# Performance work log

Hardware: AMD Instinct MI355X
Metric: run time of the kernel (lower is better)

## Reference

```python
import jax, jax.numpy as jnp
import numpy as np

# Module hyperparameters (match init_kwargs)
C = 64      # in_channels
O = 256     # out_channels
K = 3       # filter_size
SUB = 2     # subsampling
SIGMA = 1.0
SCALE = 1.0 / SIGMA ** 2
EPS = 1e-8


def setup_inputs() -> dict:
    key = jax.random.key(0)
    k1, k2 = jax.random.split(key)
    x = jax.random.normal(k1, (32, C, 64, 64), dtype=jnp.float32)
    weight = jax.random.normal(k2, (O, C * K * K), dtype=jnp.float32)
    return {"x": x, "weight": weight}


def reference(x, weight):
    # Faithful to CKNLayer.forward, but expressed as a direct convolution
    # instead of materializing the im2col (unfold) tensor:
    #   unfold -> per-patch L2 norm -> (patches/norm) @ w_norm.T
    # == conv(x, w_norm) / patch_norm,   patch_norm = sqrt(conv(x^2, ones))
    B, _, H, W = x.shape
    pad = K // 2

    # F.normalize(weight, p=2, dim=1): clamp norm at 1e-12
    w_norm = weight / jnp.maximum(
        jnp.linalg.norm(weight, axis=1, keepdims=True), 1e-12
    )
    # torch unfold orders patch features as (c, kh, kw) -> reshape matches
    w4 = w_norm.reshape(O, C, K, K)

    dn = jax.lax.conv_dimension_numbers(x.shape, w4.shape, ('NCHW', 'OIHW', 'NCHW'))
    dots = jax.lax.conv_general_dilated(
        x, w4, window_strides=(1, 1), padding=[(pad, pad), (pad, pad)],
        dimension_numbers=dn)  # [B, O, H, W]

    ones_k = jnp.ones((1, C, K, K), x.dtype)
    sq = jax.lax.conv_general_dilated(
        x * x, ones_k, window_strides=(1, 1), padding=[(pad, pad), (pad, pad)],
        dimension_numbers=dn)  # [B, 1, H, W] = sum of squares per patch
    patch_norm = jnp.sqrt(jnp.maximum(sq, 0.0)) + EPS

    # Gaussian RBF on the unit sphere: exp(scale * (cos_sim - 1))
    out = jnp.exp(SCALE * (dots / patch_norm - 1.0))  # [B, O, H, W]

    # avg_pool2d(kernel=SUB, stride=SUB), H, W divisible by SUB
    out = out.reshape(B, O, H // SUB, SUB, W // SUB, SUB).mean(axis=(3, 5))
    return out
```

## Files before the change

### kernel.cpp

```cpp
#include <hip/hip_runtime.h>
#include <hip/hip_bf16.h>

typedef __attribute__((ext_vector_type(8))) short bf16x8;
typedef __attribute__((ext_vector_type(4))) float f32x4;
typedef __attribute__((ext_vector_type(16))) float f32x16;
typedef __attribute__((ext_vector_type(4))) unsigned u32x4;

__device__ __forceinline__ unsigned bfbits(float v) {
  __hip_bfloat16 h = __float2bfloat16(v);
  return (unsigned)*reinterpret_cast<unsigned short*>(&h);
}

__device__ __forceinline__ void wnorm_one(const float* __restrict__ w,
                                          ushort* __restrict__ wt,
                                          ushort* __restrict__ wt3,
                                          int o, int c) {
  float v[9];
  float ss = 0.f;
  const float* row = w + o * 576 + c * 9;
#pragma unroll
  for (int j = 0; j < 9; ++j) { v[j] = row[j]; ss += v[j] * v[j]; }
#pragma unroll
  for (int off = 32; off > 0; off >>= 1) ss += __shfl_xor(ss, off);
  const float inv = 1.0f / fmaxf(sqrtf(ss), 1e-12f);
  const int g = o >> 5, n = o & 31;
#pragma unroll
  for (int j = 0; j < 9; ++j) {
    const ushort bv = (ushort)bfbits(v[j] * inv);
    wt[o * 576 + j * 64 + c] = bv;
    const int ks = j * 4 + (c >> 4);
    wt3[((ks * 8 + g) * 32 + n) * 16 + (c & 15)] = bv;
  }
}

__global__ void wnorm_kernel(const float* __restrict__ w,
                             ushort* __restrict__ wt,
                             ushort* __restrict__ wt3) {
  wnorm_one(w, wt, wt3, blockIdx.x, threadIdx.x);
}

__global__ __launch_bounds__(256, 8) void xprep_kernel(
    const float* __restrict__ x, ushort* __restrict__ xt,
    float* __restrict__ css, const float* __restrict__ w,
    ushort* __restrict__ wt, ushort* __restrict__ wt3) {
  __shared__ __align__(16) unsigned tile[64 * 33];
  __shared__ __align__(16) float cssp[4 * 64];
  const int t = threadIdx.x;
  if (blockIdx.y == 32) {
    wnorm_one(w, wt, wt3, blockIdx.x * 4 + (t >> 6), t & 63);
    return;
  }
  const int y = blockIdx.x, b = blockIdx.y;
  const int c = t >> 2, m = t & 3;
  const int lane = t & 63, wv = t >> 6;

  const float* src = x + (((size_t)b * 64 + c) * 64 + y) * 64 + m * 4;
  float f[16];
#pragma unroll
  for (int j4 = 0; j4 < 4; ++j4) {
    const f32x4 v = *(const f32x4*)(src + j4 * 16);
#pragma unroll
    for (int k = 0; k < 4; ++k) f[j4 * 4 + k] = v[k];
  }
  float s[16];
#pragma unroll
  for (int j = 0; j < 16; ++j) {
    float v = f[j] * f[j];
    v += __shfl_xor(v, 4);
    v += __shfl_xor(v, 8);
    v += __shfl_xor(v, 16);
    v += __shfl_xor(v, 32);
    s[j] = v;
  }
  if (lane < 4) {
#pragma unroll
    for (int j4 = 0; j4 < 4; ++j4) {
      f32x4 v = {s[j4 * 4], s[j4 * 4 + 1], s[j4 * 4 + 2], s[j4 * 4 + 3]};
      *(f32x4*)(cssp + wv * 64 + j4 * 16 + lane * 4) = v;
    }
  }
  const int parity = c & 1;
  const int c2 = c >> 1;
#pragma unroll
  for (int j = 0; j < 16; ++j) {
    const float pf = __shfl_xor(f[j], 4);
    const bool mine = parity ? (j >= 8) : (j < 8);
    if (mine) {
      const unsigned dw = parity ? (bfbits(pf) | (bfbits(f[j]) << 16))
                                 : (bfbits(f[j]) | (bfbits(pf) << 16));
      const int px = (j >> 2) * 16 + m * 4 + (j & 3);
      tile[px * 33 + c2] = dw;
    }
  }
  __syncthreads();
  {
    const int xr = t & 63, q = t >> 6;
    unsigned d[8];
#pragma unroll
    for (int i = 0; i < 8; ++i) d[i] = tile[xr * 33 + q * 8 + i];
    ushort* dst =
        xt + ((((size_t)b * 64 + y) * 8 + 2 * q) * 64 + xr) * 8;
    u32x4 v0 = {d[0], d[1], d[2], d[3]};
    u32x4 v1 = {d[4], d[5], d[6], d[7]};
    *(u32x4*)dst = v0;
    *(u32x4*)(dst + 512) = v1;
  }
  if (t < 64) {
    const float sum = cssp[t] + cssp[64 + t] + cssp[128 + t] + cssp[192 + t];
    css[((size_t)b * 64 + y) * 64 + t] = sum;
  }
}

__global__ __launch_bounds__(512, 4) void ckn_main(
    const ushort* __restrict__ xt, const float* __restrict__ css,
    const ushort* __restrict__ wt3, float* __restrict__ out) {
  __shared__ __align__(16) char smem[67328];
  char* const xs = smem;
  float* const pool = (float*)(smem + 33792);
  float* const invp = (float*)(smem + 66816);
  const int PS = 258;

  const int tid = threadIdx.x;
  const int y0 = blockIdx.x;
  const int b = blockIdx.y;

  if (tid < 128) {
    const int ry = tid >> 6, xx = tid & 63;
    const int yc = 2 * y0 + ry;
    float s = 0.f;
#pragma unroll
    for (int dy = -1; dy <= 1; ++dy) {
      const int yy = yc + dy;
      if ((unsigned)yy < 64u) s += css[((size_t)b * 64 + yy) * 64 + xx];
    }
    const float sl = __shfl_up(s, 1);
    const float sr = __shfl_down(s, 1);
    const float tot = s + ((xx > 0) ? sl : 0.f) + ((xx < 63) ? sr : 0.f);
    invp[tid] = 1.0f / (sqrtf(fmaxf(tot, 0.f)) + 1e-8f);
  }

  if (tid < 64) {
    const int r4 = tid >> 4, cb = (tid >> 1) & 7, colsel = tid & 1;
    *(f32x4*)(xs + r4 * 8448 + cb * 1056 + colsel * 65 * 16) =
        (f32x4){0.f, 0.f, 0.f, 0.f};
  }

  {
    const int l = tid & 63;
    const int w = tid >> 6;
    const ushort* srcb = xt + (((size_t)b * 64) * 8 + w) * 512 + l * 8;
#pragma unroll
    for (int r4 = 0; r4 < 4; ++r4) {
      const int y_img = 2 * y0 - 1 + r4;
      char* dst = xs + r4 * 8448 + w * 1056 + (l + 1) * 16;
      if ((unsigned)y_img < 64u) {
        const ushort* src = srcb + (size_t)y_img * 4096;
        __builtin_amdgcn_global_load_lds(
            (const __attribute__((address_space(1))) void*)src,
            (__attribute__((address_space(3))) void*)dst, 16, 0, 0);
      } else {
        *(f32x4*)dst = (f32x4){0.f, 0.f, 0.f, 0.f};
      }
    }
  }

  const int lane = tid & 63;
  const int wid = tid >> 6;
  const int wave_m = wid & 1;
  const int wave_n = wid >> 1;
  const int lane31 = lane & 31;
  const int hi = lane >> 5;

  const ushort* wb3 = wt3 + (size_t)lane31 * 16 + hi * 8;
  const int g0 = wave_n * 2;

  bf16x8 bq[2][2];
#pragma unroll
  for (int nf = 0; nf < 2; ++nf) {
    bq[0][nf] = *(const bf16x8*)(wb3 + (size_t)(0 * 8 + g0 + nf) * 512);
    bq[1][nf] = *(const bf16x8*)(wb3 + (size_t)(1 * 8 + g0 + nf) * 512);
  }

  int PH[2][3];
#pragma unroll
  for (int mf = 0; mf < 2; ++mf)
#pragma unroll
    for (int kw = 0; kw < 3; ++kw)
      PH[mf][kw] =
          (mf * 32 + lane31 + kw) * 16 + hi * 1056 + wave_m * 8448;

  __syncthreads();

  f32x16 acc[2][2];
#pragma unroll
  for (int i = 0; i < 2; ++i)
#pragma unroll
    for (int j = 0; j < 2; ++j)
#pragma unroll
      for (int e = 0; e < 16; ++e) acc[i][j][e] = 0.f;

#pragma unroll
  for (int ks = 0; ks < 36; ++ks) {
    const int t9 = ks >> 2;
    const int kh = t9 / 3, kw = t9 % 3;
    const int stepoff = kh * 8448 + (ks & 3) * 2112;
    const int cur = ks & 1;
    bf16x8 afrag[2];
#pragma unroll
    for (int mf = 0; mf < 2; ++mf)
      afrag[mf] = *(const bf16x8*)(xs + PH[mf][kw] + stepoff);
    __builtin_amdgcn_s_setprio(1);
#pragma unroll
    for (int mf = 0; mf < 2; ++mf)
#pragma unroll
      for (int nf = 0; nf < 2; ++nf)
        acc[mf][nf] = __builtin_amdgcn_mfma_f32_32x32x16_bf16(
            afrag[mf], bq[cur][nf], acc[mf][nf], 0, 0, 0);
    __builtin_amdgcn_s_setprio(0);
    if (ks + 2 < 36) {
#pragma unroll
      for (int nf = 0; nf < 2; ++nf)
        bq[cur][nf] =
            *(const bf16x8*)(wb3 + (size_t)((ks + 2) * 8 + g0 + nf) * 512);
    }
  }

  if (wave_m == 1) {
#pragma unroll
    for (int mf = 0; mf < 2; ++mf)
#pragma unroll
      for (int q = 0; q < 4; ++q) {
        const f32x4 ip = *(const f32x4*)(invp + 64 + mf * 32 + 8 * q + 4 * hi);
        const int px = mf * 16 + 4 * q + 2 * hi;
#pragma unroll
        for (int nf = 0; nf < 2; ++nf) {
          const int o = wave_n * 64 + nf * 32 + lane31;
          const float e0 = __expf(acc[mf][nf][4 * q + 0] * ip[0] - 1.f);
          const float e1 = __expf(acc[mf][nf][4 * q + 1] * ip[1] - 1.f);
          const float e2 = __expf(acc[mf][nf][4 * q + 2] * ip[2] - 1.f);
          const float e3 = __expf(acc[mf][nf][4 * q + 3] * ip[3] - 1.f);
          pool[px * PS + o] = e0 + e1;
          pool[(px + 1) * PS + o] = e2 + e3;
        }
      }
  }
  __syncthreads();
  if (wave_m == 0) {
#pragma unroll
    for (int mf = 0; mf < 2; ++mf)
#pragma unroll
      for (int q = 0; q < 4; ++q) {
        const f32x4 ip = *(const f32x4*)(invp + mf * 32 + 8 * q + 4 * hi);
        const int px = mf * 16 + 4 * q + 2 * hi;
#pragma unroll
        for (int nf = 0; nf < 2; ++nf) {
          const int o = wave_n * 64 + nf * 32 + lane31;
          const float e0 = __expf(acc[mf][nf][4 * q + 0] * ip[0] - 1.f);
          const float e1 = __expf(acc[mf][nf][4 * q + 1] * ip[1] - 1.f);
          const float e2 = __expf(acc[mf][nf][4 * q + 2] * ip[2] - 1.f);
          const float e3 = __expf(acc[mf][nf][4 * q + 3] * ip[3] - 1.f);
          pool[px * PS + o] = 0.25f * (pool[px * PS + o] + e0 + e1);
          pool[(px + 1) * PS + o] = 0.25f * (pool[(px + 1) * PS + o] + e2 + e3);
        }
      }
  }
  __syncthreads();

  const size_t obase = (((size_t)b * 256) * 32 + y0) * 32;
#pragma unroll
  for (int j = 0; j < 4; ++j) {
    const int o = j * 64 + (tid >> 3);
    const int ch = (tid & 7) * 4;
    const f32x4 v = {pool[(ch + 0) * PS + o], pool[(ch + 1) * PS + o],
                     pool[(ch + 2) * PS + o], pool[(ch + 3) * PS + o]};
    *(f32x4*)(out + obase + (size_t)o * 1024 + ch) = v;
  }
}

__global__ __launch_bounds__(512, 4) void ckn_main_v1(
    const float* __restrict__ x, const ushort* __restrict__ wt,
    float* __restrict__ out) {
  __shared__ __align__(16) char smem[43552];
  char* const xs = smem;
  float* const invp = (float*)(smem + 33792);
  float* const cs = (float*)(smem + 34304);
  float* const csp = (float*)(smem + 35360);
  float* const pool = (float*)smem;

  const int tid = threadIdx.x;
  const int y0 = blockIdx.x;
  const int b = blockIdx.y;

  if (tid < 64) {
    const int r4 = tid >> 4, colsel = (tid >> 3) & 1, cblk = tid & 7;
    const int col = colsel * 65;
    *(f32x4*)(xs + r4 * 8448 + col * 128 + cblk * 16) =
        (f32x4){0.f, 0.f, 0.f, 0.f};
  }
  {
    const int xx = tid & 63;
    const int cg = tid >> 6;
    const int col = xx + 1;
    const int sw = (cg * 16) ^ ((col & 7) << 4);
#pragma unroll
    for (int r4 = 0; r4 < 4; ++r4) {
      const int y_img = 2 * y0 - 1 + r4;
      char* dst = xs + r4 * 8448 + col * 128 + sw;
      if ((unsigned)y_img < 64u) {
        const float* src =
            x + (((size_t)b * 64 + cg * 8) * 64 + y_img) * 64 + xx;
        float ss = 0.f;
        union { bf16x8 v; ushort u[8]; } pk;
#pragma unroll
        for (int j = 0; j < 8; ++j) {
          const float f = src[(size_t)j * 4096];
          ss += f * f;
          pk.u[j] = (ushort)bfbits(f);
        }
        *(bf16x8*)dst = pk.v;
        csp[(r4 * 8 + cg) * 64 + xx] = ss;
      } else {
        *(bf16x8*)dst = (bf16x8){0, 0, 0, 0, 0, 0, 0, 0};
        csp[(r4 * 8 + cg) * 64 + xx] = 0.f;
      }
    }
  }
  __syncthreads();
  if (tid < 256) {
    const int r4 = tid >> 6, xc = tid & 63;
    float s = 0.f;
#pragma unroll
    for (int cg = 0; cg < 8; ++cg) s += csp[(r4 * 8 + cg) * 64 + xc];
    cs[r4 * 66 + xc + 1] = s;
  }
  if (tid >= 256 && tid < 264) {
    const int t = tid - 256;
    cs[(t >> 1) * 66 + (t & 1) * 65] = 0.f;
  }
  __syncthreads();
  if (tid < 128) {
    const int ry = tid >> 6, xp = tid & 63;
    float s = 0.f;
#pragma unroll
    for (int dr = 0; dr < 3; ++dr)
#pragma unroll
      for (int dc = 0; dc < 3; ++dc) s += cs[(ry + dr) * 66 + xp + dc];
    invp[tid] = 1.0f / (sqrtf(fmaxf(s, 0.f)) + 1e-8f);
  }
  __syncthreads();

  const int lane = tid & 63;
  const int wid = tid >> 6;
  const int wave_m = wid & 1;
  const int wave_n = wid >> 1;
  const int lane16 = lane & 15;
  const int klane = lane >> 4;
  const int o_base = wave_n * 64;

  f32x4 acc[4][4];
#pragma unroll
  for (int i = 0; i < 4; ++i)
#pragma unroll
    for (int j = 0; j < 4; ++j) acc[i][j] = (f32x4){0.f, 0.f, 0.f, 0.f};
  const ushort* wbase = wt + (o_base + lane16) * 576 + klane * 8;
#pragma unroll
  for (int ks = 0; ks < 18; ++ks) {
    const int t9 = ks >> 1;
    const int kh = t9 / 3, kw = t9 % 3;
    const int cb = (ks & 1) * 64 + klane * 16;
    bf16x8 bfrag[4];
#pragma unroll
    for (int fn = 0; fn < 4; ++fn)
      bfrag[fn] = *(const bf16x8*)(wbase + fn * 16 * 576 + ks * 32);
    const int r4 = wave_m + kh;
#pragma unroll
    for (int fm = 0; fm < 4; ++fm) {
      const int col = fm * 16 + lane16 + kw;
      const int addr = r4 * 8448 + col * 128 + (cb ^ ((col & 7) << 4));
      const bf16x8 afrag = *(const bf16x8*)(xs + addr);
#pragma unroll
      for (int fn = 0; fn < 4; ++fn)
        acc[fm][fn] = __builtin_amdgcn_mfma_f32_16x16x32_bf16(
            afrag, bfrag[fn], acc[fm][fn], 0, 0, 0);
    }
  }
  float ep0[4][4], ep1[4][4];
#pragma unroll
  for (int fm = 0; fm < 4; ++fm) {
    const int m = wave_m * 64 + fm * 16 + klane * 4;
    const f32x4 ip = *(const f32x4*)(invp + m);
#pragma unroll
    for (int fn = 0; fn < 4; ++fn) {
      const f32x4 v = acc[fm][fn];
      const float e0 = __expf(v[0] * ip[0] - 1.f);
      const float e1 = __expf(v[1] * ip[1] - 1.f);
      const float e2 = __expf(v[2] * ip[2] - 1.f);
      const float e3 = __expf(v[3] * ip[3] - 1.f);
      ep0[fm][fn] = e0 + e1;
      ep1[fm][fn] = e2 + e3;
    }
  }
  __syncthreads();
  if (wave_m == 1) {
#pragma unroll
    for (int fm = 0; fm < 4; ++fm) {
      const int ox = fm * 8 + klane * 2;
#pragma unroll
      for (int fn = 0; fn < 4; ++fn) {
        const int o = o_base + fn * 16 + lane16;
        *(float2*)(pool + o * 32 + ox) = make_float2(ep0[fm][fn], ep1[fm][fn]);
      }
    }
  }
  __syncthreads();
  if (wave_m == 0) {
#pragma unroll
    for (int fm = 0; fm < 4; ++fm) {
      const int ox = fm * 8 + klane * 2;
#pragma unroll
      for (int fn = 0; fn < 4; ++fn) {
        const int o = o_base + fn * 16 + lane16;
        const float2 othr = *(const float2*)(pool + o * 32 + ox);
        const float r0 = 0.25f * (ep0[fm][fn] + othr.x);
        const float r1 = 0.25f * (ep1[fm][fn] + othr.y);
        *(float2*)(out + ((((size_t)b * 256 + o) * 32 + y0) * 32 + ox)) =
            make_float2(r0, r1);
      }
    }
  }
}

extern "C" void kernel_launch(void* const* d_in, const int* in_sizes, int n_in,
                              void* d_out, int out_size, void* d_ws,
                              size_t ws_size, hipStream_t stream) {
  const float* x = (const float*)d_in[0];
  const float* w = (const float*)d_in[1];
  float* out = (float*)d_out;

  const size_t XT_BYTES = 32ull * 64 * 64 * 64 * 2;
  const size_t CSS_BYTES = 32ull * 64 * 64 * 4;
  const size_t WT_BYTES = 256ull * 576 * 2;
  const size_t NEED = XT_BYTES + CSS_BYTES + 2 * WT_BYTES;

  if (ws_size >= NEED) {
    ushort* xt = (ushort*)d_ws;
    float* css = (float*)((char*)d_ws + XT_BYTES);
    ushort* wt = (ushort*)((char*)d_ws + XT_BYTES + CSS_BYTES);
    ushort* wt3 = (ushort*)((char*)d_ws + XT_BYTES + CSS_BYTES + WT_BYTES);

    xprep_kernel<<<dim3(64, 33), dim3(256), 0, stream>>>(x, xt, css, w, wt,
                                                         wt3);
    ckn_main<<<dim3(32, 32), dim3(512), 0, stream>>>(xt, css, wt3, out);
  } else {
    ushort* wt = (ushort*)d_ws;
    ushort* wt3 = wt + 256 * 576;
    if (ws_size >= 2 * WT_BYTES) {
      wnorm_kernel<<<dim3(256), dim3(64), 0, stream>>>(w, wt, wt3);
      ckn_main_v1<<<dim3(32, 32), dim3(512), 0, stream>>>(x, wt, out);
    }
  }
}
```

Measured before the change: 64.43 us.

## Process two pooled output rows per block and reuse shared halo rows

```diff
diff --git a/kernel.cpp b/kernel.cpp
--- a/kernel.cpp
+++ b/kernel.cpp
@@ -114,19 +114,19 @@
 __global__ __launch_bounds__(512, 4) void ckn_main(
     const ushort* __restrict__ xt, const float* __restrict__ css,
     const ushort* __restrict__ wt3, float* __restrict__ out) {
-  __shared__ __align__(16) char smem[67328];
+  __shared__ __align__(16) char smem[51712];
   char* const xs = smem;
-  float* const pool = (float*)(smem + 33792);
-  float* const invp = (float*)(smem + 66816);
+  float* const pool = (float*)smem;
+  float* const invp = (float*)(smem + 50688);
   const int PS = 258;
 
   const int tid = threadIdx.x;
-  const int y0 = blockIdx.x;
+  const int yq = blockIdx.x;
   const int b = blockIdx.y;
 
-  if (tid < 128) {
+  if (tid < 256) {
     const int ry = tid >> 6, xx = tid & 63;
-    const int yc = 2 * y0 + ry;
+    const int yc = 4 * yq + ry;
     float s = 0.f;
 #pragma unroll
     for (int dy = -1; dy <= 1; ++dy) {
@@ -139,9 +139,9 @@
     invp[tid] = 1.0f / (sqrtf(fmaxf(tot, 0.f)) + 1e-8f);
   }
 
-  if (tid < 64) {
-    const int r4 = tid >> 4, cb = (tid >> 1) & 7, colsel = tid & 1;
-    *(f32x4*)(xs + r4 * 8448 + cb * 1056 + colsel * 65 * 16) =
+  if (tid < 96) {
+    const int r6 = tid >> 4, cb = (tid >> 1) & 7, colsel = tid & 1;
+    *(f32x4*)(xs + r6 * 8448 + cb * 1056 + colsel * 65 * 16) =
         (f32x4){0.f, 0.f, 0.f, 0.f};
   }
 
@@ -150,9 +150,9 @@
     const int w = tid >> 6;
     const ushort* srcb = xt + (((size_t)b * 64) * 8 + w) * 512 + l * 8;
 #pragma unroll
-    for (int r4 = 0; r4 < 4; ++r4) {
-      const int y_img = 2 * y0 - 1 + r4;
-      char* dst = xs + r4 * 8448 + w * 1056 + (l + 1) * 16;
+    for (int r6 = 0; r6 < 6; ++r6) {
+      const int y_img = 4 * yq - 1 + r6;
+      char* dst = xs + r6 * 8448 + w * 1056 + (l + 1) * 16;
       if ((unsigned)y_img < 64u) {
         const ushort* src = srcb + (size_t)y_img * 4096;
         __builtin_amdgcn_global_load_lds(
@@ -166,7 +166,7 @@
 
   const int lane = tid & 63;
   const int wid = tid >> 6;
-  const int wave_m = wid & 1;
+  const int wxh = wid & 1;
   const int wave_n = wid >> 1;
   const int lane31 = lane & 31;
   const int hi = lane >> 5;
@@ -181,99 +181,100 @@
     bq[1][nf] = *(const bf16x8*)(wb3 + (size_t)(1 * 8 + g0 + nf) * 512);
   }
 
-  int PH[2][3];
-#pragma unroll
-  for (int mf = 0; mf < 2; ++mf)
-#pragma unroll
-    for (int kw = 0; kw < 3; ++kw)
-      PH[mf][kw] =
-          (mf * 32 + lane31 + kw) * 16 + hi * 1056 + wave_m * 8448;
-
-  __syncthreads();
-
-  f32x16 acc[2][2];
-#pragma unroll
-  for (int i = 0; i < 2; ++i)
-#pragma unroll
-    for (int j = 0; j < 2; ++j)
-#pragma unroll
-      for (int e = 0; e < 16; ++e) acc[i][j][e] = 0.f;
-
-#pragma unroll
-  for (int ks = 0; ks < 36; ++ks) {
-    const int t9 = ks >> 2;
-    const int kh = t9 / 3, kw = t9 % 3;
-    const int stepoff = kh * 8448 + (ks & 3) * 2112;
-    const int cur = ks & 1;
-    bf16x8 afrag[2];
-#pragma unroll
-    for (int mf = 0; mf < 2; ++mf)
-      afrag[mf] = *(const bf16x8*)(xs + PH[mf][kw] + stepoff);
-    __builtin_amdgcn_s_setprio(1);
-#pragma unroll
-    for (int mf = 0; mf < 2; ++mf)
-#pragma unroll
-      for (int nf = 0; nf < 2; ++nf)
-        acc[mf][nf] = __builtin_amdgcn_mfma_f32_32x32x16_bf16(
-            afrag[mf], bq[cur][nf], acc[mf][nf], 0, 0, 0);
-    __builtin_amdgcn_s_setprio(0);
-    if (ks + 2 < 36) {
-#pragma unroll
-      for (int nf = 0; nf < 2; ++nf)
-        bq[cur][nf] =
-            *(const bf16x8*)(wb3 + (size_t)((ks + 2) * 8 + g0 + nf) * 512);
-    }
-  }
-
-  if (wave_m == 1) {
-#pragma unroll
-    for (int mf = 0; mf < 2; ++mf)
-#pragma unroll
-      for (int q = 0; q < 4; ++q) {
-        const f32x4 ip = *(const f32x4*)(invp + 64 + mf * 32 + 8 * q + 4 * hi);
-        const int px = mf * 16 + 4 * q + 2 * hi;
-#pragma unroll
-        for (int nf = 0; nf < 2; ++nf) {
-          const int o = wave_n * 64 + nf * 32 + lane31;
-          const float e0 = __expf(acc[mf][nf][4 * q + 0] * ip[0] - 1.f);
-          const float e1 = __expf(acc[mf][nf][4 * q + 1] * ip[1] - 1.f);
-          const float e2 = __expf(acc[mf][nf][4 * q + 2] * ip[2] - 1.f);
-          const float e3 = __expf(acc[mf][nf][4 * q + 3] * ip[3] - 1.f);
-          pool[px * PS + o] = e0 + e1;
-          pool[(px + 1) * PS + o] = e2 + e3;
-        }
-      }
-  }
-  __syncthreads();
-  if (wave_m == 0) {
-#pragma unroll
-    for (int mf = 0; mf < 2; ++mf)
-#pragma unroll
-      for (int q = 0; q < 4; ++q) {
-        const f32x4 ip = *(const f32x4*)(invp + mf * 32 + 8 * q + 4 * hi);
-        const int px = mf * 16 + 4 * q + 2 * hi;
-#pragma unroll
-        for (int nf = 0; nf < 2; ++nf) {
-          const int o = wave_n * 64 + nf * 32 + lane31;
-          const float e0 = __expf(acc[mf][nf][4 * q + 0] * ip[0] - 1.f);
-          const float e1 = __expf(acc[mf][nf][4 * q + 1] * ip[1] - 1.f);
-          const float e2 = __expf(acc[mf][nf][4 * q + 2] * ip[2] - 1.f);
-          const float e3 = __expf(acc[mf][nf][4 * q + 3] * ip[3] - 1.f);
-          pool[px * PS + o] = 0.25f * (pool[px * PS + o] + e0 + e1);
-          pool[(px + 1) * PS + o] = 0.25f * (pool[(px + 1) * PS + o] + e2 + e3);
-        }
-      }
-  }
-  __syncthreads();
-
-  const size_t obase = (((size_t)b * 256) * 32 + y0) * 32;
-#pragma unroll
-  for (int j = 0; j < 4; ++j) {
-    const int o = j * 64 + (tid >> 3);
-    const int ch = (tid & 7) * 4;
-    const f32x4 v = {pool[(ch + 0) * PS + o], pool[(ch + 1) * PS + o],
-                     pool[(ch + 2) * PS + o], pool[(ch + 3) * PS + o]};
-    *(f32x4*)(out + obase + (size_t)o * 1024 + ch) = v;
+  int PH[3];
+#pragma unroll
+  for (int kw = 0; kw < 3; ++kw)
+    PH[kw] = (wxh * 32 + lane31 + kw) * 16 + hi * 1056;
+
+  __syncthreads();
+
+#pragma unroll
+  for (int p = 0; p < 2; ++p) {
+    f32x16 acc[2][2];
+#pragma unroll
+    for (int i = 0; i < 2; ++i)
+#pragma unroll
+      for (int j = 0; j < 2; ++j)
+#pragma unroll
+        for (int e = 0; e < 16; ++e) acc[i][j][e] = 0.f;
+
+#pragma unroll
+    for (int ks = 0; ks < 36; ++ks) {
+      const int t9 = ks >> 2;
+      const int kh = t9 / 3, kw = t9 % 3;
+      const int off = (2 * p + kh) * 8448 + (ks & 3) * 2112;
+      const int cur = ks & 1;
+      bf16x8 afrag[2];
+#pragma unroll
+      for (int mf = 0; mf < 2; ++mf)
+        afrag[mf] = *(const bf16x8*)(xs + PH[kw] + off + mf * 8448);
+      __builtin_amdgcn_s_setprio(1);
+#pragma unroll
+      for (int mf = 0; mf < 2; ++mf)
+#pragma unroll
+        for (int nf = 0; nf < 2; ++nf)
+          acc[mf][nf] = __builtin_amdgcn_mfma_f32_32x32x16_bf16(
+              afrag[mf], bq[cur][nf], acc[mf][nf], 0, 0, 0);
+      __builtin_amdgcn_s_setprio(0);
+      const int nxt = (ks + 2 < 36) ? (ks + 2) : (p == 0 ? ks - 34 : -1);
+      if (nxt >= 0) {
+#pragma unroll
+        for (int nf = 0; nf < 2; ++nf)
+          bq[cur][nf] =
+              *(const bf16x8*)(wb3 + (size_t)(nxt * 8 + g0 + nf) * 512);
+      }
+    }
+
+    __syncthreads();
+
+    float pv[4][2][2];
+#pragma unroll
+    for (int q = 0; q < 4; ++q) {
+      const f32x4 ip0 =
+          *(const f32x4*)(invp + (2 * p + 0) * 64 + wxh * 32 + 8 * q + 4 * hi);
+      const f32x4 ip1 =
+          *(const f32x4*)(invp + (2 * p + 1) * 64 + wxh * 32 + 8 * q + 4 * hi);
+#pragma unroll
+      for (int nf = 0; nf < 2; ++nf) {
+        const float a0 = __expf(acc[0][nf][4 * q + 0] * ip0[0] - 1.f) +
+                         __expf(acc[0][nf][4 * q + 1] * ip0[1] - 1.f);
+        const float a1 = __expf(acc[0][nf][4 * q + 2] * ip0[2] - 1.f) +
+                         __expf(acc[0][nf][4 * q + 3] * ip0[3] - 1.f);
+        const float b0 = __expf(acc[1][nf][4 * q + 0] * ip1[0] - 1.f) +
+                         __expf(acc[1][nf][4 * q + 1] * ip1[1] - 1.f);
+        const float b1 = __expf(acc[1][nf][4 * q + 2] * ip1[2] - 1.f) +
+                         __expf(acc[1][nf][4 * q + 3] * ip1[3] - 1.f);
+        pv[q][nf][0] = 0.25f * (a0 + b0);
+        pv[q][nf][1] = 0.25f * (a1 + b1);
+      }
+    }
+
+#pragma unroll
+    for (int h = 0; h < 2; ++h) {
+      if (wxh == h) {
+#pragma unroll
+        for (int q = 0; q < 4; ++q)
+#pragma unroll
+          for (int nf = 0; nf < 2; ++nf) {
+            const int o = wave_n * 64 + nf * 32 + lane31;
+            pool[(4 * q + 2 * hi + 0) * PS + o] = pv[q][nf][0];
+            pool[(4 * q + 2 * hi + 1) * PS + o] = pv[q][nf][1];
+          }
+      }
+      __syncthreads();
+#pragma unroll
+      for (int j = 0; j < 2; ++j) {
+        const int sidx = tid + 512 * j;
+        const int o = sidx >> 2, q4 = sidx & 3;
+        const f32x4 v = {pool[(q4 * 4 + 0) * PS + o],
+                         pool[(q4 * 4 + 1) * PS + o],
+                         pool[(q4 * 4 + 2) * PS + o],
+                         pool[(q4 * 4 + 3) * PS + o]};
+        *(f32x4*)(out + (((size_t)b * 256 + o) * 32 + 2 * yq + p) * 32 +
+                  h * 16 + q4 * 4) = v;
+      }
+      __syncthreads();
+    }
   }
 }
 
@@ -450,7 +451,7 @@
 
     xprep_kernel<<<dim3(64, 33), dim3(256), 0, stream>>>(x, xt, css, w, wt,
                                                          wt3);
-    ckn_main<<<dim3(32, 32), dim3(512), 0, stream>>>(xt, css, wt3, out);
+    ckn_main<<<dim3(16, 32), dim3(512), 0, stream>>>(xt, css, wt3, out);
   } else {
     ushort* wt = (ushort*)d_ws;
     ushort* wt3 = wt + 256 * 576;
```

After: 118.4 us. 1.84x slower.
